# Kernel optimization log

Hardware: AMD Instinct MI355X
Metric: run time of the kernel (lower is better)

The kernel has to match this reference:

```python
import jax, jax.numpy as jnp
import numpy as np

N_NODES = 100000
N_EDGES = 1600000
IN_DIM, HID_DIM, OUT_DIM = 64, 64, 16


def setup_inputs() -> dict:
    key = jax.random.key(0)
    k1, k2, k3, k4 = jax.random.split(key, 4)
    x = jax.random.normal(k1, (N_NODES, IN_DIM), dtype=jnp.float32)
    edge_index = jax.random.randint(k2, (2, N_EDGES), 0, N_NODES, dtype=jnp.int64)
    W1 = jax.random.normal(k3, (IN_DIM, HID_DIM), dtype=jnp.float32) * (1.0 / np.sqrt(IN_DIM))
    b1 = jnp.zeros((HID_DIM,), dtype=jnp.float32)
    W2 = jax.random.normal(k4, (HID_DIM, OUT_DIM), dtype=jnp.float32) * (1.0 / np.sqrt(HID_DIM))
    b2 = jnp.zeros((OUT_DIM,), dtype=jnp.float32)
    return {"x": x, "edge_index": edge_index, "W1": W1, "b1": b1, "W2": W2, "b2": b2}


def gcn_conv(x, src, dst, W, b, num_nodes):
    """GCNConv: h = D^{-1/2} (A+I) D^{-1/2} (x W) + b, edge-list form with self-loops already appended."""
    # symmetric degree normalization (degree counted at destination, incl. self-loops)
    deg = jax.ops.segment_sum(jnp.ones_like(dst, dtype=x.dtype), dst, num_segments=num_nodes)
    dinv = jnp.where(deg > 0, jax.lax.rsqrt(deg), 0.0)
    norm = dinv[src] * dinv[dst]                      # [E+N]
    h = x @ W                                         # [N, H] project first (fewer flops on edges)
    msg = h[src] * norm[:, None]                      # gather + scale, [E+N, H]
    out = jax.ops.segment_sum(msg, dst, num_segments=num_nodes)  # scatter-add
    return out + b


def reference(x, edge_index, W1, b1, W2, b2):
    num_nodes = x.shape[0]
    loop = jnp.arange(num_nodes, dtype=edge_index.dtype)
    src = jnp.concatenate([edge_index[0], loop])      # add self-loops once, reuse for both layers
    dst = jnp.concatenate([edge_index[1], loop])
    h = gcn_conv(x, src, dst, W1, b1, num_nodes)
    h = jax.nn.relu(h)
    # F.dropout(training=self.training): eval mode -> identity
    out = gcn_conv(h, src, dst, W2, b2, num_nodes)
    return out
```

## Files before the change

### kernel.cpp

```cpp
#include <hip/hip_runtime.h>

constexpr int N_NODES = 100000;
constexpr int F1 = 64;
constexpr int F2 = 16;
constexpr int SH = 7;
constexpr int NPB = 128;
constexpr int NBINS = (N_NODES + NPB - 1) / NPB;
constexpr int CAPB = 2560;
constexpr int TILE = 4096;
constexpr int GSTRIDE = 16;

static __device__ __forceinline__ unsigned short f2bf(float f) {
    unsigned int u = __float_as_uint(f);
    unsigned int r = (u + 0x7fffu + ((u >> 16) & 1u)) >> 16;
    return (unsigned short)r;
}
static __device__ __forceinline__ float bf2f(unsigned short b) {
    return __uint_as_float(((unsigned int)b) << 16);
}

__global__ __launch_bounds__(512) void k_bin(const int* __restrict__ src,
                                             const int* __restrict__ dst, int E,
                                             unsigned int* __restrict__ gcnt,
                                             unsigned int* __restrict__ entries) {
    __shared__ unsigned int cnt[NBINS];
    __shared__ unsigned int cur[NBINS];
    int tid = threadIdx.x;
    int base = blockIdx.x * TILE;
    int end = min(base + TILE, E);
    for (int i = tid; i < NBINS; i += 512) cnt[i] = 0;
    __syncthreads();
    for (int e = base + tid; e < end; e += 512) atomicAdd(&cnt[dst[e] >> SH], 1u);
    __syncthreads();
    for (int i = tid; i < NBINS; i += 512) {
        unsigned int c = cnt[i];
        cur[i] = (unsigned int)i * CAPB + (c ? atomicAdd(&gcnt[i * GSTRIDE], c) : 0u);
    }
    __syncthreads();
    for (int e = base + tid; e < end; e += 512) {
        int d = dst[e];
        int s = src[e];
        int bb = d >> SH;
        unsigned int p = atomicAdd(&cur[bb], 1u);
        if (p - (unsigned int)bb * CAPB < CAPB)
            entries[p] = (unsigned int)s | ((unsigned int)(d & (NPB - 1)) << 17);
    }
}

__global__ __launch_bounds__(256) void k_dinvb(const unsigned int* __restrict__ gcnt,
                                               const unsigned int* __restrict__ entries,
                                               float* __restrict__ dinv) {
    __shared__ unsigned int ncnt[NPB];
    int tid = threadIdx.x;
    int b = blockIdx.x;
    unsigned int cntE = gcnt[b * GSTRIDE]; if (cntE > CAPB) cntE = CAPB;
    unsigned int base = (unsigned int)b * CAPB;
    if (tid < NPB) ncnt[tid] = 0;
    __syncthreads();
    for (unsigned int e = tid; e < cntE; e += 256)
        atomicAdd(&ncnt[entries[base + e] >> 17], 1u);
    __syncthreads();
    if (tid < NPB) {
        int node = b * NPB + tid;
        if (node < N_NODES) dinv[node] = rsqrtf((float)(ncnt[tid] + 1u));
    }
}

__global__ __launch_bounds__(256) void k_xw1(const float* __restrict__ x,
                                             const float* __restrict__ W,
                                             const float* __restrict__ dinv,
                                             unsigned short* __restrict__ hs) {
    constexpr int XS = 68;
    __shared__ float Ws[64 * 64];
    __shared__ float xs[64 * XS];
    int tid = threadIdx.x;
    int r0 = blockIdx.x * 64;
    for (int i = tid; i < 1024; i += 256) {
        int k = i >> 4, c4 = (i & 15) << 2;
        *(float4*)&Ws[k * 64 + c4] = *(const float4*)&W[k * 64 + c4];
    }
    for (int i = tid; i < 1024; i += 256) {
        int rr = i >> 4, c4 = (i & 15) << 2;
        int r = r0 + rr;
        float4 v = make_float4(0.f, 0.f, 0.f, 0.f);
        if (r < N_NODES) v = *(const float4*)&x[(size_t)r * 64 + c4];
        *(float4*)&xs[rr * XS + c4] = v;
    }
    __syncthreads();
    int tx = tid & 15, ty = tid >> 4;
    int c0 = tx << 2, rb = ty << 2;
    float acc[4][4] = {};
#pragma unroll 8
    for (int k = 0; k < 64; ++k) {
        float4 w = *(float4*)&Ws[k * 64 + c0];
        float x0 = xs[(rb + 0) * XS + k];
        float x1 = xs[(rb + 1) * XS + k];
        float x2 = xs[(rb + 2) * XS + k];
        float x3 = xs[(rb + 3) * XS + k];
        acc[0][0] += x0 * w.x; acc[0][1] += x0 * w.y; acc[0][2] += x0 * w.z; acc[0][3] += x0 * w.w;
        acc[1][0] += x1 * w.x; acc[1][1] += x1 * w.y; acc[1][2] += x1 * w.z; acc[1][3] += x1 * w.w;
        acc[2][0] += x2 * w.x; acc[2][1] += x2 * w.y; acc[2][2] += x2 * w.z; acc[2][3] += x2 * w.w;
        acc[3][0] += x3 * w.x; acc[3][1] += x3 * w.y; acc[3][2] += x3 * w.z; acc[3][3] += x3 * w.w;
    }
#pragma unroll
    for (int i = 0; i < 4; ++i) {
        int r = r0 + rb + i;
        if (r >= N_NODES) break;
        float dv = dinv[r];
        ushort4 p;
        p.x = f2bf(acc[i][0] * dv);
        p.y = f2bf(acc[i][1] * dv);
        p.z = f2bf(acc[i][2] * dv);
        p.w = f2bf(acc[i][3] * dv);
        *(ushort4*)&hs[(size_t)r * 64 + c0] = p;
    }
}

__global__ __launch_bounds__(1024) void k_agg1f(const unsigned int* __restrict__ gcnt,
                                                const unsigned int* __restrict__ entries,
                                                const unsigned short* __restrict__ hs,
                                                const float* __restrict__ dinv,
                                                unsigned short* __restrict__ out1) {
    __shared__ unsigned int ncnt[NPB];
    __shared__ unsigned int noff[NPB + 1];
    __shared__ unsigned int cur[NPB];
    __shared__ unsigned int sl[CAPB];
    int tid = threadIdx.x;
    int b = blockIdx.x;
    unsigned int cntE = gcnt[b * GSTRIDE]; if (cntE > CAPB) cntE = CAPB;
    unsigned int base = (unsigned int)b * CAPB;
    if (tid < NPB) ncnt[tid] = 0;
    __syncthreads();
    for (unsigned int e = tid; e < cntE; e += 1024)
        atomicAdd(&ncnt[entries[base + e] >> 17], 1u);
    __syncthreads();
    if (tid < NPB) cur[tid] = ncnt[tid];
    __syncthreads();
    for (int ofs = 1; ofs < NPB; ofs <<= 1) {
        unsigned int v = (tid < NPB && tid >= ofs) ? cur[tid - ofs] : 0u;
        __syncthreads();
        if (tid < NPB) cur[tid] += v;
        __syncthreads();
    }
    if (tid < NPB) noff[tid + 1] = cur[tid];
    if (tid == 0) noff[0] = 0;
    __syncthreads();
    if (tid < NPB) cur[tid] = noff[tid];
    __syncthreads();
    for (unsigned int e = tid; e < cntE; e += 1024) {
        unsigned int v = entries[base + e];
        unsigned int p = atomicAdd(&cur[v >> 17], 1u);
        sl[p] = v & 0x1FFFFu;
    }
    __syncthreads();
    int wid = tid >> 6, k = tid & 63;
    for (int n = wid; n < NPB; n += 16) {
        int node = b * NPB + n;
        if (node >= N_NODES) break;
        unsigned int j = noff[n], jend = noff[n + 1];
        float acc = bf2f(hs[(size_t)node * 64 + k]);
        for (; j + 8 <= jend; j += 8) {
            unsigned int s0 = sl[j], s1 = sl[j + 1], s2 = sl[j + 2], s3 = sl[j + 3];
            unsigned int s4 = sl[j + 4], s5 = sl[j + 5], s6 = sl[j + 6], s7 = sl[j + 7];
            float a0 = bf2f(hs[(size_t)s0 * 64 + k]);
            float a1 = bf2f(hs[(size_t)s1 * 64 + k]);
            float a2 = bf2f(hs[(size_t)s2 * 64 + k]);
            float a3 = bf2f(hs[(size_t)s3 * 64 + k]);
            float a4 = bf2f(hs[(size_t)s4 * 64 + k]);
            float a5 = bf2f(hs[(size_t)s5 * 64 + k]);
            float a6 = bf2f(hs[(size_t)s6 * 64 + k]);
            float a7 = bf2f(hs[(size_t)s7 * 64 + k]);
            acc += ((a0 + a1) + (a2 + a3)) + ((a4 + a5) + (a6 + a7));
        }
        for (; j + 4 <= jend; j += 4) {
            unsigned int s0 = sl[j], s1 = sl[j + 1], s2 = sl[j + 2], s3 = sl[j + 3];
            float a0 = bf2f(hs[(size_t)s0 * 64 + k]);
            float a1 = bf2f(hs[(size_t)s1 * 64 + k]);
            float a2 = bf2f(hs[(size_t)s2 * 64 + k]);
            float a3 = bf2f(hs[(size_t)s3 * 64 + k]);
            acc += (a0 + a1) + (a2 + a3);
        }
        for (; j < jend; ++j) acc += bf2f(hs[(size_t)sl[j] * 64 + k]);
        out1[(size_t)node * 64 + k] = f2bf(acc * dinv[node]);
    }
}

__global__ __launch_bounds__(256) void k_xw2(const unsigned short* __restrict__ out1,
                                             const float* __restrict__ b1,
                                             const float* __restrict__ W2,
                                             const float* __restrict__ dinv,
                                             unsigned short* __restrict__ h2s) {
    constexpr int RS = 66;
    __shared__ float Ws[64 * 16];
    __shared__ float rs[128 * RS];
    __shared__ float b1s[64];
    int tid = threadIdx.x;
    int r0 = blockIdx.x * 128;
    if (tid < 64) b1s[tid] = b1[tid];
    for (int i = tid; i < 256; i += 256)
        *(float4*)&Ws[i * 4] = *(const float4*)&W2[i * 4];
    __syncthreads();
    for (int i = tid; i < 2048; i += 256) {
        int rr = i >> 4, c4 = (i & 15) << 2;
        int r = r0 + rr;
        float v0 = 0.f, v1 = 0.f, v2 = 0.f, v3 = 0.f;
        if (r < N_NODES) {
            ushort4 u = *(const ushort4*)&out1[(size_t)r * 64 + c4];
            v0 = fmaxf(bf2f(u.x) + b1s[c4 + 0], 0.f);
            v1 = fmaxf(bf2f(u.y) + b1s[c4 + 1], 0.f);
            v2 = fmaxf(bf2f(u.z) + b1s[c4 + 2], 0.f);
            v3 = fmaxf(bf2f(u.w) + b1s[c4 + 3], 0.f);
        }
        float* pp = &rs[rr * RS + c4];
        pp[0] = v0; pp[1] = v1; pp[2] = v2; pp[3] = v3;
    }
    __syncthreads();
    int tx = tid & 3, ty = tid >> 2;
    int c0 = tx << 2, rb = ty << 1;
    float acc[2][4] = {};
#pragma unroll 8
    for (int k = 0; k < 64; ++k) {
        float4 w = *(float4*)&Ws[k * 16 + c0];
        float x0 = rs[(rb + 0) * RS + k];
        float x1 = rs[(rb + 1) * RS + k];
        acc[0][0] += x0 * w.x; acc[0][1] += x0 * w.y; acc[0][2] += x0 * w.z; acc[0][3] += x0 * w.w;
        acc[1][0] += x1 * w.x; acc[1][1] += x1 * w.y; acc[1][2] += x1 * w.z; acc[1][3] += x1 * w.w;
    }
#pragma unroll
    for (int i = 0; i < 2; ++i) {
        int r = r0 + rb + i;
        if (r >= N_NODES) break;
        float dv = dinv[r];
        ushort4 p;
        p.x = f2bf(acc[i][0] * dv);
        p.y = f2bf(acc[i][1] * dv);
        p.z = f2bf(acc[i][2] * dv);
        p.w = f2bf(acc[i][3] * dv);
        *(ushort4*)&h2s[(size_t)r * 16 + c0] = p;
    }
}

__global__ __launch_bounds__(1024) void k_agg2f(const unsigned int* __restrict__ gcnt,
                                                const unsigned int* __restrict__ entries,
                                                const unsigned short* __restrict__ h2s,
                                                const float* __restrict__ dinv,
                                                const float* __restrict__ b2,
                                                float* __restrict__ out) {
    __shared__ unsigned int ncnt[NPB];
    __shared__ unsigned int noff[NPB + 1];
    __shared__ unsigned int cur[NPB];
    __shared__ unsigned int sl[CAPB];
    int tid = threadIdx.x;
    int b = blockIdx.x;
    unsigned int cntE = gcnt[b * GSTRIDE]; if (cntE > CAPB) cntE = CAPB;
    unsigned int base = (unsigned int)b * CAPB;
    if (tid < NPB) ncnt[tid] = 0;
    __syncthreads();
    for (unsigned int e = tid; e < cntE; e += 1024)
        atomicAdd(&ncnt[entries[base + e] >> 17], 1u);
    __syncthreads();
    if (tid < NPB) cur[tid] = ncnt[tid];
    __syncthreads();
    for (int ofs = 1; ofs < NPB; ofs <<= 1) {
        unsigned int v = (tid < NPB && tid >= ofs) ? cur[tid - ofs] : 0u;
        __syncthreads();
        if (tid < NPB) cur[tid] += v;
        __syncthreads();
    }
    if (tid < NPB) noff[tid + 1] = cur[tid];
    if (tid == 0) noff[0] = 0;
    __syncthreads();
    if (tid < NPB) cur[tid] = noff[tid];
    __syncthreads();
    for (unsigned int e = tid; e < cntE; e += 1024) {
        unsigned int v = entries[base + e];
        unsigned int p = atomicAdd(&cur[v >> 17], 1u);
        sl[p] = v & 0x1FFFFu;
    }
    __syncthreads();
    int wid = tid >> 6, lane = tid & 63;
    int k = lane & 15, esub = lane >> 4;
    for (int n = wid; n < NPB; n += 16) {
        int node = b * NPB + n;
        if (node >= N_NODES) break;
        unsigned int j0 = noff[n], jend = noff[n + 1];
        float acc = 0.0f;
        unsigned int j = j0 + esub;
        for (; j + 4 < jend; j += 8) {
            float a = bf2f(h2s[(size_t)sl[j] * 16 + k]);
            float c = bf2f(h2s[(size_t)sl[j + 4] * 16 + k]);
            acc += a + c;
        }
        if (j < jend) acc += bf2f(h2s[(size_t)sl[j] * 16 + k]);
        acc += __shfl_xor(acc, 16);
        acc += __shfl_xor(acc, 32);
        if (lane < 16)
            out[(size_t)node * 16 + k] = (acc + bf2f(h2s[(size_t)node * 16 + k])) * dinv[node] + b2[k];
    }
}

static inline size_t align256(size_t x) { return (x + 255) & ~size_t(255); }

extern "C" void kernel_launch(void* const* d_in, const int* in_sizes, int n_in,
                              void* d_out, int out_size, void* d_ws, size_t ws_size,
                              hipStream_t stream) {
    const float* x  = (const float*)d_in[0];
    const int* edge = (const int*)d_in[1];
    const float* W1 = (const float*)d_in[2];
    const float* b1 = (const float*)d_in[3];
    const float* W2 = (const float*)d_in[4];
    const float* b2 = (const float*)d_in[5];
    float* out = (float*)d_out;

    const int E = in_sizes[1] / 2;
    const int* src = edge;
    const int* dst = edge + E;

    char* ws = (char*)d_ws;
    size_t o = 0;
    unsigned int* gcnt    = (unsigned int*)(ws + o); o += align256((size_t)NBINS * GSTRIDE * 4);
    float* dinv           = (float*)(ws + o);        o += align256((size_t)N_NODES * 4);
    unsigned int* entries = (unsigned int*)(ws + o); o += align256((size_t)NBINS * CAPB * 4);
    unsigned short* hs    = (unsigned short*)(ws + o); o += align256((size_t)N_NODES * F1 * 2);
    unsigned short* out1  = (unsigned short*)(ws + o); o += align256((size_t)N_NODES * F1 * 2);
    unsigned short* h2s   = (unsigned short*)(ws + o); o += align256((size_t)N_NODES * F2 * 2);

    hipMemsetAsync(gcnt, 0, (size_t)NBINS * GSTRIDE * 4, stream);

    k_bin<<<(E + TILE - 1) / TILE, 512, 0, stream>>>(src, dst, E, gcnt, entries);
    k_dinvb<<<NBINS, 256, 0, stream>>>(gcnt, entries, dinv);

    k_xw1<<<(N_NODES + 63) / 64, 256, 0, stream>>>(x, W1, dinv, hs);
    k_agg1f<<<NBINS, 1024, 0, stream>>>(gcnt, entries, hs, dinv, out1);

    k_xw2<<<(N_NODES + 127) / 128, 256, 0, stream>>>(out1, b1, W2, dinv, h2s);
    k_agg2f<<<NBINS, 1024, 0, stream>>>(gcnt, entries, h2s, dinv, b2, out);
}
```

Before: 147.9 us.

## Fuse degree computation into first projection and reuse sorted CSR in second aggregation

The separate inverse-degree kernel is removed. Its per-bin degree counting now runs inside the first projection kernel, which is retiled to 128 rows per block with 512 threads so each block matches one destination bin. The first aggregation kernel writes its per-node sorted source lists and offsets back to global memory, so the second aggregation only loads them instead of recounting, rescanning and resorting. This trades one kernel launch and a redundant counting-sort pass for extra global writes of the sorted lists and offsets.

```diff
diff --git a/kernel.cpp b/kernel.cpp
--- a/kernel.cpp
+++ b/kernel.cpp
@@ -47,44 +47,43 @@
     }
 }
 
-__global__ __launch_bounds__(256) void k_dinvb(const unsigned int* __restrict__ gcnt,
-                                               const unsigned int* __restrict__ entries,
-                                               float* __restrict__ dinv) {
-    __shared__ unsigned int ncnt[NPB];
-    int tid = threadIdx.x;
-    int b = blockIdx.x;
-    unsigned int cntE = gcnt[b * GSTRIDE]; if (cntE > CAPB) cntE = CAPB;
-    unsigned int base = (unsigned int)b * CAPB;
-    if (tid < NPB) ncnt[tid] = 0;
-    __syncthreads();
-    for (unsigned int e = tid; e < cntE; e += 256)
-        atomicAdd(&ncnt[entries[base + e] >> 17], 1u);
-    __syncthreads();
-    if (tid < NPB) {
-        int node = b * NPB + tid;
-        if (node < N_NODES) dinv[node] = rsqrtf((float)(ncnt[tid] + 1u));
-    }
-}
-
-__global__ __launch_bounds__(256) void k_xw1(const float* __restrict__ x,
+__global__ __launch_bounds__(512) void k_xw1(const float* __restrict__ x,
                                              const float* __restrict__ W,
-                                             const float* __restrict__ dinv,
+                                             const unsigned int* __restrict__ gcnt,
+                                             const unsigned int* __restrict__ entries,
+                                             float* __restrict__ dinv,
                                              unsigned short* __restrict__ hs) {
     constexpr int XS = 68;
     __shared__ float Ws[64 * 64];
-    __shared__ float xs[64 * XS];
-    int tid = threadIdx.x;
-    int r0 = blockIdx.x * 64;
-    for (int i = tid; i < 1024; i += 256) {
+    __shared__ float xs[128 * XS];
+    __shared__ unsigned int ncnt[NPB];
+    __shared__ float dinvs[NPB];
+    int tid = threadIdx.x;
+    int b = blockIdx.x;
+    int r0 = b * NPB;
+    for (int i = tid; i < 1024; i += 512) {
         int k = i >> 4, c4 = (i & 15) << 2;
         *(float4*)&Ws[k * 64 + c4] = *(const float4*)&W[k * 64 + c4];
     }
-    for (int i = tid; i < 1024; i += 256) {
+    for (int i = tid; i < 2048; i += 512) {
         int rr = i >> 4, c4 = (i & 15) << 2;
         int r = r0 + rr;
         float4 v = make_float4(0.f, 0.f, 0.f, 0.f);
         if (r < N_NODES) v = *(const float4*)&x[(size_t)r * 64 + c4];
         *(float4*)&xs[rr * XS + c4] = v;
+    }
+    if (tid < NPB) ncnt[tid] = 0;
+    __syncthreads();
+    unsigned int cntE = gcnt[b * GSTRIDE]; if (cntE > CAPB) cntE = CAPB;
+    unsigned int ebase = (unsigned int)b * CAPB;
+    for (unsigned int e = tid; e < cntE; e += 512)
+        atomicAdd(&ncnt[entries[ebase + e] >> 17], 1u);
+    __syncthreads();
+    if (tid < NPB) {
+        int node = r0 + tid;
+        float dv = rsqrtf((float)(ncnt[tid] + 1u));
+        dinvs[tid] = dv;
+        if (node < N_NODES) dinv[node] = dv;
     }
     __syncthreads();
     int tx = tid & 15, ty = tid >> 4;
@@ -106,7 +105,7 @@
     for (int i = 0; i < 4; ++i) {
         int r = r0 + rb + i;
         if (r >= N_NODES) break;
-        float dv = dinv[r];
+        float dv = dinvs[rb + i];
         ushort4 p;
         p.x = f2bf(acc[i][0] * dv);
         p.y = f2bf(acc[i][1] * dv);
@@ -117,7 +116,8 @@
 }
 
 __global__ __launch_bounds__(1024) void k_agg1f(const unsigned int* __restrict__ gcnt,
-                                                const unsigned int* __restrict__ entries,
+                                                unsigned int* __restrict__ entries,
+                                                unsigned int* __restrict__ noffg,
                                                 const unsigned short* __restrict__ hs,
                                                 const float* __restrict__ dinv,
                                                 unsigned short* __restrict__ out1) {
@@ -153,6 +153,8 @@
         sl[p] = v & 0x1FFFFu;
     }
     __syncthreads();
+    for (unsigned int e = tid; e < cntE; e += 1024) entries[base + e] = sl[e];
+    if (tid <= NPB) noffg[b * (NPB + 1) + tid] = noff[tid];
     int wid = tid >> 6, k = tid & 63;
     for (int n = wid; n < NPB; n += 16) {
         int node = b * NPB + n;
@@ -241,42 +243,20 @@
 }
 
 __global__ __launch_bounds__(1024) void k_agg2f(const unsigned int* __restrict__ gcnt,
-                                                const unsigned int* __restrict__ entries,
+                                                const unsigned int* __restrict__ sorted,
+                                                const unsigned int* __restrict__ noffg,
                                                 const unsigned short* __restrict__ h2s,
                                                 const float* __restrict__ dinv,
                                                 const float* __restrict__ b2,
                                                 float* __restrict__ out) {
-    __shared__ unsigned int ncnt[NPB];
     __shared__ unsigned int noff[NPB + 1];
-    __shared__ unsigned int cur[NPB];
     __shared__ unsigned int sl[CAPB];
     int tid = threadIdx.x;
     int b = blockIdx.x;
     unsigned int cntE = gcnt[b * GSTRIDE]; if (cntE > CAPB) cntE = CAPB;
     unsigned int base = (unsigned int)b * CAPB;
-    if (tid < NPB) ncnt[tid] = 0;
-    __syncthreads();
-    for (unsigned int e = tid; e < cntE; e += 1024)
-        atomicAdd(&ncnt[entries[base + e] >> 17], 1u);
-    __syncthreads();
-    if (tid < NPB) cur[tid] = ncnt[tid];
-    __syncthreads();
-    for (int ofs = 1; ofs < NPB; ofs <<= 1) {
-        unsigned int v = (tid < NPB && tid >= ofs) ? cur[tid - ofs] : 0u;
-        __syncthreads();
-        if (tid < NPB) cur[tid] += v;
-        __syncthreads();
-    }
-    if (tid < NPB) noff[tid + 1] = cur[tid];
-    if (tid == 0) noff[0] = 0;
-    __syncthreads();
-    if (tid < NPB) cur[tid] = noff[tid];
-    __syncthreads();
-    for (unsigned int e = tid; e < cntE; e += 1024) {
-        unsigned int v = entries[base + e];
-        unsigned int p = atomicAdd(&cur[v >> 17], 1u);
-        sl[p] = v & 0x1FFFFu;
-    }
+    if (tid <= NPB) noff[tid] = noffg[b * (NPB + 1) + tid];
+    for (unsigned int e = tid; e < cntE; e += 1024) sl[e] = sorted[base + e];
     __syncthreads();
     int wid = tid >> 6, lane = tid & 63;
     int k = lane & 15, esub = lane >> 4;
@@ -321,6 +301,7 @@
     unsigned int* gcnt    = (unsigned int*)(ws + o); o += align256((size_t)NBINS * GSTRIDE * 4);
     float* dinv           = (float*)(ws + o);        o += align256((size_t)N_NODES * 4);
     unsigned int* entries = (unsigned int*)(ws + o); o += align256((size_t)NBINS * CAPB * 4);
+    unsigned int* noffg   = (unsigned int*)(ws + o); o += align256((size_t)NBINS * (NPB + 1) * 4);
     unsigned short* hs    = (unsigned short*)(ws + o); o += align256((size_t)N_NODES * F1 * 2);
     unsigned short* out1  = (unsigned short*)(ws + o); o += align256((size_t)N_NODES * F1 * 2);
     unsigned short* h2s   = (unsigned short*)(ws + o); o += align256((size_t)N_NODES * F2 * 2);
@@ -328,11 +309,10 @@
     hipMemsetAsync(gcnt, 0, (size_t)NBINS * GSTRIDE * 4, stream);
 
     k_bin<<<(E + TILE - 1) / TILE, 512, 0, stream>>>(src, dst, E, gcnt, entries);
-    k_dinvb<<<NBINS, 256, 0, stream>>>(gcnt, entries, dinv);
-
-    k_xw1<<<(N_NODES + 63) / 64, 256, 0, stream>>>(x, W1, dinv, hs);
-    k_agg1f<<<NBINS, 1024, 0, stream>>>(gcnt, entries, hs, dinv, out1);
+
+    k_xw1<<<NBINS, 512, 0, stream>>>(x, W1, gcnt, entries, dinv, hs);
+    k_agg1f<<<NBINS, 1024, 0, stream>>>(gcnt, entries, noffg, hs, dinv, out1);
 
     k_xw2<<<(N_NODES + 127) / 128, 256, 0, stream>>>(out1, b1, W2, dinv, h2s);
-    k_agg2f<<<NBINS, 1024, 0, stream>>>(gcnt, entries, h2s, dinv, b2, out);
-}
+    k_agg2f<<<NBINS, 1024, 0, stream>>>(gcnt, entries, noffg, h2s, dinv, b2, out);
+}
```

After: 144.4 us. 2.3% less time.
